# Performance work log

Measured on AMD Instinct MI355X. Metric: run time of the kernel, lower is better.

## Reference

```python
import jax, jax.numpy as jnp
import numpy as np

DIM = 384
B = 256
EPS = 1e-5


def _conv_replicate(x, W, pad):
    # x: [B,C,H,W], W: [O,I,kh,kw]; replicate (edge) padding then VALID conv
    x = jnp.pad(x, ((0, 0), (0, 0), (pad, pad), (pad, pad)), mode='edge')
    return jax.lax.conv_general_dilated(
        x, W, window_strides=(1, 1), padding='VALID',
        dimension_numbers=('NCHW', 'OIHW', 'NCHW'))


def _bn(x, g, b, m, v):
    scale = (g / jnp.sqrt(v + EPS))[None, :, None, None]
    return (x - m[None, :, None, None]) * scale + b[None, :, None, None]


def _clip_features(target, bbox):
    # target: [B, 576, C] -> vectorized per-sample crop + nearest resize to 12x12
    bb = bbox * 24.0
    x, y, w, h = bb[:, 0], bb[:, 1], bb[:, 2], bb[:, 3]
    l = (w + h) / 2
    l = jnp.sqrt((w + l) * (h + l))
    x_min = jnp.clip(jnp.ceil(x - l / 2), 0, 23).astype(jnp.int32)
    y_min = jnp.clip(jnp.ceil(y - l / 2), 0, 23).astype(jnp.int32)
    x_max = jnp.clip(jnp.trunc(x + l / 2), 0, 23).astype(jnp.int32)
    y_max = jnp.clip(jnp.trunc(y + l / 2), 0, 23).astype(jnp.int32)
    i12 = jnp.arange(12, dtype=jnp.int32)
    # nearest-neighbor source index: crop_start + floor(i * crop_size / 12)
    rows = y_min[:, None] + (i12[None, :] * (y_max - y_min)[:, None]) // 12  # [B,12]
    cols = x_min[:, None] + (i12[None, :] * (x_max - x_min)[:, None]) // 12  # [B,12]
    rows = jnp.clip(rows, 0, 23)
    cols = jnp.clip(cols, 0, 23)
    Bn, N, C = target.shape
    tflat = jnp.transpose(target, (0, 2, 1))  # [B, C, 576] (row-major 24x24)
    idx = rows[:, :, None] * 24 + cols[:, None, :]  # [B,12,12]
    idx = jnp.broadcast_to(idx.reshape(Bn, 1, 144), (Bn, C, 144))
    out = jnp.take_along_axis(tflat, idx, axis=2)  # [B, C, 144]
    return out.reshape(Bn, C, 12, 12)


def setup_inputs() -> dict:
    key = jax.random.key(0)
    ks = jax.random.split(key, 8)
    temp = jax.random.normal(ks[0], (B, 144, DIM), dtype=jnp.float32)
    target = jax.random.normal(ks[1], (B, 576, DIM), dtype=jnp.float32)
    u = jax.random.uniform(ks[2], (B, 4), dtype=jnp.float32)
    # centers in [0.3,0.7], sizes in [0.25,0.45] -> always a valid non-empty crop
    bbox = jnp.concatenate([0.3 + 0.4 * u[:, :2], 0.25 + 0.2 * u[:, 2:]], axis=1)
    W1 = jax.random.normal(ks[3], (DIM, DIM, 5, 5), dtype=jnp.float32) * 0.02
    W2 = jax.random.normal(ks[4], (DIM, DIM, 3, 3), dtype=jnp.float32) * 0.05
    g1 = jnp.ones((DIM,), jnp.float32)
    b1 = jnp.zeros((DIM,), jnp.float32)
    m1 = jax.random.normal(ks[5], (DIM,), dtype=jnp.float32) * 0.1
    v1 = jnp.ones((DIM,), jnp.float32)
    g2 = jnp.ones((DIM,), jnp.float32)
    b2 = jnp.zeros((DIM,), jnp.float32)
    m2 = jax.random.normal(ks[6], (DIM,), dtype=jnp.float32) * 0.1
    v2 = jnp.ones((DIM,), jnp.float32)
    return dict(temp=temp, target=target, bbox=bbox, W1=W1, g1=g1, b1=b1,
                m1=m1, v1=v1, W2=W2, g2=g2, b2=b2, m2=m2, v2=v2)


def reference(temp, target, bbox, W1, g1, b1, m1, v1, W2, g2, b2, m2, v2):
    ta = _clip_features(target, bbox)  # [B, C, 12, 12]
    h1 = jax.nn.leaky_relu(_bn(_conv_replicate(ta, W1, 2), g1, b1, m1, v1), 0.01)
    h2 = jax.nn.leaky_relu(_bn(_conv_replicate(h1, W2, 1), g2, b2, m2, v2), 0.01)
    Bn, N, C = temp.shape
    t = jnp.transpose(temp, (0, 2, 1)).reshape(Bn, C, 12, 12)
    out = (t + h2).reshape(Bn, C, 144)
    return jnp.transpose(out, (0, 2, 1))  # [B, 144, C]
```

## Files before the change

### kernel.cpp

```cpp
#include <hip/hip_runtime.h>
#include <math.h>

#define NBATCH 256
#define CDIM   384

typedef __attribute__((ext_vector_type(4))) float  f32x4;
typedef __attribute__((ext_vector_type(8))) __bf16 bf16x8;

__device__ __forceinline__ void load16(const void* g, void* l) {
    __builtin_amdgcn_global_load_lds(
        (const __attribute__((address_space(1))) void*)g,
        (__attribute__((address_space(3))) void*)l, 16, 0, 0);
}

__global__ __launch_bounds__(256) void gather_bf16(
    const float* __restrict__ target,
    const float* __restrict__ bbox,
    __bf16* __restrict__ ta)
{
    const int b = blockIdx.x, t = threadIdx.x;
    __shared__ int pos[144];

    if (t < 144) {
        const float bx0 = bbox[b * 4 + 0] * 24.f;
        const float by0 = bbox[b * 4 + 1] * 24.f;
        const float bw  = bbox[b * 4 + 2] * 24.f;
        const float bh  = bbox[b * 4 + 3] * 24.f;
        const float l0 = (bw + bh) * 0.5f;
        const float l  = sqrtf((bw + l0) * (bh + l0));
        const int xmin = (int)fminf(fmaxf(ceilf (bx0 - l * 0.5f), 0.f), 23.f);
        const int ymin = (int)fminf(fmaxf(ceilf (by0 - l * 0.5f), 0.f), 23.f);
        const int xmax = (int)fminf(fmaxf(truncf(bx0 + l * 0.5f), 0.f), 23.f);
        const int ymax = (int)fminf(fmaxf(truncf(by0 + l * 0.5f), 0.f), 23.f);
        const int i = t / 12, j = t % 12;
        int r = ymin + (i * (ymax - ymin)) / 12;
        int c = xmin + (j * (xmax - xmin)) / 12;
        r = min(max(r, 0), 23);
        c = min(max(c, 0), 23);
        pos[t] = r * 24 + c;
    }
    __syncthreads();

    const float* tb  = target + (size_t)b * 576 * 384;
    __bf16*      tab = ta     + (size_t)b * 144 * 384;
    for (int idx = t; idx < 144 * 384; idx += 256) {
        const int p = idx / 384, c = idx - p * 384;
        tab[idx] = (__bf16)tb[(size_t)pos[p] * 384 + c];
    }
}

__global__ __launch_bounds__(256) void prep_w(
    const float* __restrict__ W, __bf16* __restrict__ Wt, int taps)
{
    const int idx = blockIdx.x * 256 + threadIdx.x;
    const int total = 384 * 384 * taps;
    if (idx >= total) return;
    const int oc  = idx / (384 * taps);
    const int rem = idx - oc * 384 * taps;
    const int tap = rem / 384;
    const int ic  = rem - tap * 384;
    Wt[idx] = (__bf16)W[((size_t)oc * 384 + ic) * taps + tap];
}

template <int TAPS, int KW, int PAD, bool RESID>
__global__ __launch_bounds__(256) void conv_mfma(
    const __bf16* __restrict__ A,
    const __bf16* __restrict__ Wt,
    const float* __restrict__ gg, const float* __restrict__ bb,
    const float* __restrict__ mm, const float* __restrict__ vv,
    const float* __restrict__ temp,
    void* __restrict__ outp)
{
    const int K  = TAPS * 384;
    const int m0 = blockIdx.x * 128;
    const int n0 = blockIdx.y * 128;
    const int t  = threadIdx.x;
    const int lane  = t & 63, w = t >> 6;
    const int wm    = (w & 1) * 64, wn = (w >> 1) * 64;
    const int col16 = lane & 15,  quad = lane >> 4;

    __shared__ __bf16 As[128 * 32];
    __shared__ __bf16 Bs[128 * 32];

    const int r0 = t >> 2, kg = t & 3;
    const int mrow0 = m0 + r0, mrow1 = m0 + r0 + 64;
    const int b0 = mrow0 / 144, p0 = mrow0 - b0 * 144;
    const int b1 = mrow1 / 144, p1 = mrow1 - b1 * 144;
    const int y0 = p0 / 12, x0 = p0 - y0 * 12;
    const int y1 = p1 / 12, x1 = p1 - y1 * 12;
    const __bf16* Ab0 = A + (size_t)b0 * 144 * 384 + kg * 8;
    const __bf16* Ab1 = A + (size_t)b1 * 144 * 384 + kg * 8;
    const __bf16* Bp0 = Wt + (size_t)(n0 + r0)      * K + kg * 8;
    const __bf16* Bp1 = Wt + (size_t)(n0 + r0 + 64) * K + kg * 8;

    f32x4 acc[4][4];
#pragma unroll
    for (int mi = 0; mi < 4; ++mi)
#pragma unroll
        for (int ni = 0; ni < 4; ++ni)
            acc[mi][ni] = (f32x4){0.f, 0.f, 0.f, 0.f};

    for (int tap = 0; tap < TAPS; ++tap) {
        const int ky = tap / KW - PAD, kx = tap % KW - PAD;
        const int sy0 = min(max(y0 + ky, 0), 11), sx0 = min(max(x0 + kx, 0), 11);
        const int sy1 = min(max(y1 + ky, 0), 11), sx1 = min(max(x1 + kx, 0), 11);
        const __bf16* aP0 = Ab0 + (size_t)(sy0 * 12 + sx0) * 384;
        const __bf16* aP1 = Ab1 + (size_t)(sy1 * 12 + sx1) * 384;
        const __bf16* bP0 = Bp0 + (size_t)tap * 384;
        const __bf16* bP1 = Bp1 + (size_t)tap * 384;

#pragma unroll
        for (int j = 0; j < 12; ++j) {
            __syncthreads();
            load16(aP0 + j * 32, &As[t * 8]);
            load16(aP1 + j * 32, &As[(t + 256) * 8]);
            load16(bP0 + j * 32, &Bs[t * 8]);
            load16(bP1 + j * 32, &Bs[(t + 256) * 8]);
            __syncthreads();

            bf16x8 av[4], bv[4];
#pragma unroll
            for (int mi = 0; mi < 4; ++mi)
                av[mi] = *(const bf16x8*)&As[(wm + mi * 16 + col16) * 32 + quad * 8];
#pragma unroll
            for (int ni = 0; ni < 4; ++ni)
                bv[ni] = *(const bf16x8*)&Bs[(wn + ni * 16 + col16) * 32 + quad * 8];
#pragma unroll
            for (int mi = 0; mi < 4; ++mi)
#pragma unroll
                for (int ni = 0; ni < 4; ++ni)
                    acc[mi][ni] = __builtin_amdgcn_mfma_f32_16x16x32_bf16(
                        av[mi], bv[ni], acc[mi][ni], 0, 0, 0);
        }
    }

#pragma unroll
    for (int ni = 0; ni < 4; ++ni) {
        const int gn = n0 + wn + ni * 16 + col16;
        const float scale = gg[gn] * rsqrtf(vv[gn] + 1e-5f);
        const float shift = bb[gn] - mm[gn] * scale;
        if (!RESID) {
            __bf16* h1 = (__bf16*)outp;
#pragma unroll
            for (int mi = 0; mi < 4; ++mi) {
                const int gm = m0 + wm + mi * 16 + quad * 4;
#pragma unroll
                for (int r = 0; r < 4; ++r) {
                    float v = acc[mi][ni][r] * scale + shift;
                    v = (v >= 0.f) ? v : 0.01f * v;
                    h1[(size_t)(gm + r) * 384 + gn] = (__bf16)v;
                }
            }
        } else {
            float* outF = (float*)outp;
#pragma unroll
            for (int mi = 0; mi < 4; ++mi) {
                const int gm = m0 + wm + mi * 16 + quad * 4;
#pragma unroll
                for (int r = 0; r < 4; ++r) {
                    float v = acc[mi][ni][r] * scale + shift;
                    v = (v >= 0.f) ? v : 0.01f * v;
                    outF[(size_t)(gm + r) * 384 + gn] =
                        temp[(size_t)(gm + r) * 384 + gn] + v;
                }
            }
        }
    }
}

extern "C" void kernel_launch(void* const* d_in, const int* in_sizes, int n_in,
                              void* d_out, int out_size, void* d_ws, size_t ws_size,
                              hipStream_t stream) {
    const float* temp   = (const float*)d_in[0];
    const float* target = (const float*)d_in[1];
    const float* bbox   = (const float*)d_in[2];
    const float* W1     = (const float*)d_in[3];
    const float* g1     = (const float*)d_in[4];
    const float* b1     = (const float*)d_in[5];
    const float* m1     = (const float*)d_in[6];
    const float* v1     = (const float*)d_in[7];
    const float* W2     = (const float*)d_in[8];
    const float* g2     = (const float*)d_in[9];
    const float* b2     = (const float*)d_in[10];
    const float* m2     = (const float*)d_in[11];
    const float* v2     = (const float*)d_in[12];
    float* out = (float*)d_out;

    __bf16* ta  = (__bf16*)d_ws;
    __bf16* h1  = ta  + (size_t)NBATCH * 144 * CDIM;
    __bf16* Wt1 = h1  + (size_t)NBATCH * 144 * CDIM;
    __bf16* Wt2 = Wt1 + (size_t)CDIM * 25 * CDIM;

    prep_w<<<dim3((CDIM * CDIM * 25 + 255) / 256), dim3(256), 0, stream>>>(W1, Wt1, 25);
    prep_w<<<dim3((CDIM * CDIM * 9  + 255) / 256), dim3(256), 0, stream>>>(W2, Wt2, 9);
    gather_bf16<<<dim3(NBATCH), dim3(256), 0, stream>>>(target, bbox, ta);

    conv_mfma<25, 5, 2, false><<<dim3(288, 3), dim3(256), 0, stream>>>(
        ta, Wt1, g1, b1, m1, v1, nullptr, (void*)h1);
    conv_mfma<9, 3, 1, true><<<dim3(288, 3), dim3(256), 0, stream>>>(
        h1, Wt2, g2, b2, m2, v2, temp, (void*)out);
}
```

Baseline: 986.9 us.

## Double-buffer conv LDS tiles, swizzle LDS layout, vectorize gather and weight prep

```diff
diff --git a/kernel.cpp b/kernel.cpp
--- a/kernel.cpp
+++ b/kernel.cpp
@@ -6,6 +6,7 @@
 
 typedef __attribute__((ext_vector_type(4))) float  f32x4;
 typedef __attribute__((ext_vector_type(8))) __bf16 bf16x8;
+typedef __attribute__((ext_vector_type(4))) __bf16 bf16x4;
 
 __device__ __forceinline__ void load16(const void* g, void* l) {
     __builtin_amdgcn_global_load_lds(
@@ -43,27 +44,34 @@
 
     const float* tb  = target + (size_t)b * 576 * 384;
     __bf16*      tab = ta     + (size_t)b * 144 * 384;
-    for (int idx = t; idx < 144 * 384; idx += 256) {
-        const int p = idx / 384, c = idx - p * 384;
-        tab[idx] = (__bf16)tb[(size_t)pos[p] * 384 + c];
-    }
-}
-
+    for (int idx = t; idx < 144 * 96; idx += 256) {
+        const int p = idx / 96, c4 = idx - p * 96;
+        const float4 v = *(const float4*)&tb[(size_t)pos[p] * 384 + c4 * 4];
+        bf16x4 o = { (__bf16)v.x, (__bf16)v.y, (__bf16)v.z, (__bf16)v.w };
+        *(bf16x4*)&tab[(size_t)p * 384 + c4 * 4] = o;
+    }
+}
+
+template <int TAPS>
 __global__ __launch_bounds__(256) void prep_w(
-    const float* __restrict__ W, __bf16* __restrict__ Wt, int taps)
+    const float* __restrict__ W, __bf16* __restrict__ Wt)
 {
-    const int idx = blockIdx.x * 256 + threadIdx.x;
-    const int total = 384 * 384 * taps;
-    if (idx >= total) return;
-    const int oc  = idx / (384 * taps);
-    const int rem = idx - oc * 384 * taps;
-    const int tap = rem / 384;
-    const int ic  = rem - tap * 384;
-    Wt[idx] = (__bf16)W[((size_t)oc * 384 + ic) * taps + tap];
+    const int K = TAPS * 384;
+    __shared__ float ws[TAPS * 384];
+    const int oc = blockIdx.x;
+    const float* src = W + (size_t)oc * K;
+    for (int i = threadIdx.x; i < K; i += 256) ws[i] = src[i];
+    __syncthreads();
+    __bf16* dst = Wt + (size_t)oc * K;
+    for (int i = threadIdx.x; i < K; i += 256) {
+        const int tap = i / 384;
+        const int ic  = i - tap * 384;
+        dst[i] = (__bf16)ws[ic * TAPS + tap];
+    }
 }
 
 template <int TAPS, int KW, int PAD, bool RESID>
-__global__ __launch_bounds__(256) void conv_mfma(
+__global__ __launch_bounds__(256, 3) void conv_mfma(
     const __bf16* __restrict__ A,
     const __bf16* __restrict__ Wt,
     const float* __restrict__ gg, const float* __restrict__ bb,
@@ -72,6 +80,7 @@
     void* __restrict__ outp)
 {
     const int K  = TAPS * 384;
+    const int IT = TAPS * 12;
     const int m0 = blockIdx.x * 128;
     const int n0 = blockIdx.y * 128;
     const int t  = threadIdx.x;
@@ -79,10 +88,11 @@
     const int wm    = (w & 1) * 64, wn = (w >> 1) * 64;
     const int col16 = lane & 15,  quad = lane >> 4;
 
-    __shared__ __bf16 As[128 * 32];
-    __shared__ __bf16 Bs[128 * 32];
-
-    const int r0 = t >> 2, kg = t & 3;
+    __shared__ __bf16 As0[128 * 32], As1[128 * 32];
+    __shared__ __bf16 Bs0[128 * 32], Bs1[128 * 32];
+
+    const int r0   = t >> 2, slot = t & 3;
+    const int kg   = slot ^ ((r0 >> 1) & 3);
     const int mrow0 = m0 + r0, mrow1 = m0 + r0 + 64;
     const int b0 = mrow0 / 144, p0 = mrow0 - b0 * 144;
     const int b1 = mrow1 / 144, p1 = mrow1 - b1 * 144;
@@ -90,8 +100,18 @@
     const int y1 = p1 / 12, x1 = p1 - y1 * 12;
     const __bf16* Ab0 = A + (size_t)b0 * 144 * 384 + kg * 8;
     const __bf16* Ab1 = A + (size_t)b1 * 144 * 384 + kg * 8;
-    const __bf16* Bp0 = Wt + (size_t)(n0 + r0)      * K + kg * 8;
-    const __bf16* Bp1 = Wt + (size_t)(n0 + r0 + 64) * K + kg * 8;
+
+    int offA[4], offB[4];
+#pragma unroll
+    for (int mi = 0; mi < 4; ++mi) {
+        const int r = wm + mi * 16 + col16;
+        offA[mi] = r * 32 + (quad ^ ((r >> 1) & 3)) * 8;
+    }
+#pragma unroll
+    for (int ni = 0; ni < 4; ++ni) {
+        const int r = wn + ni * 16 + col16;
+        offB[ni] = r * 32 + (quad ^ ((r >> 1) & 3)) * 8;
+    }
 
     f32x4 acc[4][4];
 #pragma unroll
@@ -100,38 +120,63 @@
         for (int ni = 0; ni < 4; ++ni)
             acc[mi][ni] = (f32x4){0.f, 0.f, 0.f, 0.f};
 
-    for (int tap = 0; tap < TAPS; ++tap) {
-        const int ky = tap / KW - PAD, kx = tap % KW - PAD;
-        const int sy0 = min(max(y0 + ky, 0), 11), sx0 = min(max(x0 + kx, 0), 11);
-        const int sy1 = min(max(y1 + ky, 0), 11), sx1 = min(max(x1 + kx, 0), 11);
-        const __bf16* aP0 = Ab0 + (size_t)(sy0 * 12 + sx0) * 384;
-        const __bf16* aP1 = Ab1 + (size_t)(sy1 * 12 + sx1) * 384;
-        const __bf16* bP0 = Bp0 + (size_t)tap * 384;
-        const __bf16* bP1 = Bp1 + (size_t)tap * 384;
-
-#pragma unroll
-        for (int j = 0; j < 12; ++j) {
-            __syncthreads();
-            load16(aP0 + j * 32, &As[t * 8]);
-            load16(aP1 + j * 32, &As[(t + 256) * 8]);
-            load16(bP0 + j * 32, &Bs[t * 8]);
-            load16(bP1 + j * 32, &Bs[(t + 256) * 8]);
-            __syncthreads();
-
-            bf16x8 av[4], bv[4];
-#pragma unroll
-            for (int mi = 0; mi < 4; ++mi)
-                av[mi] = *(const bf16x8*)&As[(wm + mi * 16 + col16) * 32 + quad * 8];
+    int jn = 0, tapn = 0;
+    const __bf16* aT0;
+    const __bf16* aT1;
+    {
+        const int sy0 = min(max(y0 - PAD, 0), 11), sx0 = min(max(x0 - PAD, 0), 11);
+        const int sy1 = min(max(y1 - PAD, 0), 11), sx1 = min(max(x1 - PAD, 0), 11);
+        aT0 = Ab0 + (size_t)(sy0 * 12 + sx0) * 384;
+        aT1 = Ab1 + (size_t)(sy1 * 12 + sx1) * 384;
+    }
+    const __bf16* bT0 = Wt + (size_t)(n0 + r0)      * K + kg * 8;
+    const __bf16* bT1 = Wt + (size_t)(n0 + r0 + 64) * K + kg * 8;
+
+    auto issue = [&](__bf16* SA, __bf16* SB) {
+        load16(aT0 + jn * 32, &SA[t * 8]);
+        load16(aT1 + jn * 32, &SA[(t + 256) * 8]);
+        load16(bT0 + jn * 32, &SB[t * 8]);
+        load16(bT1 + jn * 32, &SB[(t + 256) * 8]);
+    };
+    auto advance = [&]() {
+        if (++jn == 12) {
+            jn = 0;
+            ++tapn;
+            if (tapn < TAPS) {
+                const int ky = tapn / KW - PAD, kx = tapn % KW - PAD;
+                const int sy0 = min(max(y0 + ky, 0), 11), sx0 = min(max(x0 + kx, 0), 11);
+                const int sy1 = min(max(y1 + ky, 0), 11), sx1 = min(max(x1 + kx, 0), 11);
+                aT0 = Ab0 + (size_t)(sy0 * 12 + sx0) * 384;
+                aT1 = Ab1 + (size_t)(sy1 * 12 + sx1) * 384;
+                bT0 += 384;
+                bT1 += 384;
+            }
+        }
+    };
+    auto mfma_step = [&](const __bf16* SA, const __bf16* SB, bool do_issue,
+                         __bf16* NA, __bf16* NB_) {
+        __syncthreads();
+        bf16x8 av[4], bv[4];
+#pragma unroll
+        for (int mi = 0; mi < 4; ++mi) av[mi] = *(const bf16x8*)&SA[offA[mi]];
+#pragma unroll
+        for (int ni = 0; ni < 4; ++ni) bv[ni] = *(const bf16x8*)&SB[offB[ni]];
+        if (do_issue) issue(NA, NB_);
+#pragma unroll
+        for (int mi = 0; mi < 4; ++mi)
 #pragma unroll
             for (int ni = 0; ni < 4; ++ni)
-                bv[ni] = *(const bf16x8*)&Bs[(wn + ni * 16 + col16) * 32 + quad * 8];
-#pragma unroll
-            for (int mi = 0; mi < 4; ++mi)
-#pragma unroll
-                for (int ni = 0; ni < 4; ++ni)
-                    acc[mi][ni] = __builtin_amdgcn_mfma_f32_16x16x32_bf16(
-                        av[mi], bv[ni], acc[mi][ni], 0, 0, 0);
-        }
+                acc[mi][ni] = __builtin_amdgcn_mfma_f32_16x16x32_bf16(
+                    av[mi], bv[ni], acc[mi][ni], 0, 0, 0);
+    };
+
+    issue(As0, Bs0);
+
+    for (int it2 = 0; it2 < IT; it2 += 2) {
+        advance();
+        mfma_step(As0, Bs0, true, As1, Bs1);
+        advance();
+        mfma_step(As1, Bs1, it2 + 2 < IT, As0, Bs0);
     }
 
 #pragma unroll
@@ -191,8 +236,8 @@
     __bf16* Wt1 = h1  + (size_t)NBATCH * 144 * CDIM;
     __bf16* Wt2 = Wt1 + (size_t)CDIM * 25 * CDIM;
 
-    prep_w<<<dim3((CDIM * CDIM * 25 + 255) / 256), dim3(256), 0, stream>>>(W1, Wt1, 25);
-    prep_w<<<dim3((CDIM * CDIM * 9  + 255) / 256), dim3(256), 0, stream>>>(W2, Wt2, 9);
+    prep_w<25><<<dim3(CDIM), dim3(256), 0, stream>>>(W1, Wt1);
+    prep_w<9><<<dim3(CDIM), dim3(256), 0, stream>>>(W2, Wt2);
     gather_bf16<<<dim3(NBATCH), dim3(256), 0, stream>>>(target, bbox, ta);
 
     conv_mfma<25, 5, 2, false><<<dim3(288, 3), dim3(256), 0, stream>>>(
```

After: 912.6 us. 7.5% less time.
